# Optimization experiments

Hardware: AMD Instinct MI355X
Metric: run time of the kernel (lower is better)

Reference implementation:

```python
import jax, jax.numpy as jnp
import numpy as np

N_NODES = 100000
N_EDGES = 1000000
HID = 128


def setup_inputs() -> dict:
    key = jax.random.key(0)
    ks = jax.random.split(key, 8)
    z = jax.random.normal(ks[0], (N_NODES, HID), dtype=jnp.float32)
    edge_index = jax.random.randint(ks[1], (2, N_EDGES), 0, N_NODES, dtype=jnp.int64)
    # Linear params: W stored as [out, in] like torch; init ~ kaiming-uniform-ish scale
    W1 = jax.random.normal(ks[2], (256, 2 * HID), dtype=jnp.float32) * (1.0 / np.sqrt(2 * HID))
    b1 = jnp.zeros((256,), dtype=jnp.float32)
    W2 = jax.random.normal(ks[3], (64, 256), dtype=jnp.float32) * (1.0 / np.sqrt(256))
    b2 = jnp.zeros((64,), dtype=jnp.float32)
    W3 = jax.random.normal(ks[4], (1, 64), dtype=jnp.float32) * (1.0 / np.sqrt(64))
    b3 = jnp.zeros((1,), dtype=jnp.float32)
    return {"z": z, "edge_index": edge_index, "W1": W1, "b1": b1,
            "W2": W2, "b2": b2, "W3": W3, "b3": b3}


def reference(z, edge_index, W1, b1, W2, b2, W3, b3):
    # gather src/dst node embeddings and concat -> [E, 2*HID]
    src = z[edge_index[0]]
    dst = z[edge_index[1]]
    edge_feats = jnp.concatenate([src, dst], axis=1)
    # 3-layer MLP with leaky_relu(0.2); dropout is identity in eval mode
    h = jax.nn.leaky_relu(edge_feats @ W1.T + b1, negative_slope=0.2)
    h = jax.nn.leaky_relu(h @ W2.T + b2, negative_slope=0.2)
    return h @ W3.T + b3  # [E, 1]
```

## Files before the change

kernel.cpp:

```cpp
#include <hip/hip_runtime.h>
#include <hip/hip_bf16.h>

typedef __attribute__((ext_vector_type(8))) short bf16x8;
typedef __attribute__((ext_vector_type(4))) float f32x4;

#define HID    128
#define KDIM   256
#define MT     64

__device__ __forceinline__ unsigned short f2bf(float x) {
    unsigned int u = __float_as_uint(x);
    u += 0x7FFFu + ((u >> 16) & 1u);
    return (unsigned short)(u >> 16);
}
__device__ __forceinline__ int pack2(float a, float b) {
    return (int)f2bf(a) | ((int)f2bf(b) << 16);
}
__device__ __forceinline__ float lrelu(float x) { return fmaxf(x, 0.2f * x); }

__global__ void convert_all_kernel(const float* __restrict__ z,
                                   const float* __restrict__ W1,
                                   const float* __restrict__ W2,
                                   unsigned short* __restrict__ zb,
                                   unsigned short* __restrict__ w1b,
                                   unsigned short* __restrict__ w2b,
                                   int nz4, int nw14, int nw24) {
    int total = nz4 + nw14 + nw24;
    for (int i = blockIdx.x * blockDim.x + threadIdx.x; i < total;
         i += gridDim.x * blockDim.x) {
        const float4* src;
        unsigned short* dst;
        int j;
        if (i < nz4)             { src = (const float4*)z;  dst = zb;  j = i; }
        else if (i < nz4 + nw14) { src = (const float4*)W1; dst = w1b; j = i - nz4; }
        else                     { src = (const float4*)W2; dst = w2b; j = i - nz4 - nw14; }
        float4 v = src[j];
        ushort4 o;
        o.x = f2bf(v.x); o.y = f2bf(v.y); o.z = f2bf(v.z); o.w = f2bf(v.w);
        *(ushort4*)(dst + (size_t)j * 4) = o;
    }
}

__global__ void convert_w_kernel(const float* __restrict__ W1,
                                 const float* __restrict__ W2,
                                 unsigned short* __restrict__ w1b,
                                 unsigned short* __restrict__ w2b,
                                 int nw14, int nw24) {
    int i = blockIdx.x * blockDim.x + threadIdx.x;
    if (i >= nw14 + nw24) return;
    const float4* src;
    unsigned short* dst;
    int j;
    if (i < nw14) { src = (const float4*)W1; dst = w1b; j = i; }
    else          { src = (const float4*)W2; dst = w2b; j = i - nw14; }
    float4 v = src[j];
    ushort4 o;
    o.x = f2bf(v.x); o.y = f2bf(v.y); o.z = f2bf(v.z); o.w = f2bf(v.w);
    *(ushort4*)(dst + (size_t)j * 4) = o;
}

template <bool ZB>
__global__ __launch_bounds__(256, 4)
void disc_kernel(const float* __restrict__ z,
                 const unsigned short* __restrict__ zb,
                 const int* __restrict__ ei,
                 const unsigned short* __restrict__ w1b,
                 const float* __restrict__ b1,
                 const unsigned short* __restrict__ w2b,
                 const float* __restrict__ b2,
                 const float* __restrict__ W3,
                 const float* __restrict__ b3,
                 float* __restrict__ out, int E) {
    __shared__ __align__(16) unsigned char smem[32768];

    const int tid  = threadIdx.x;
    const int wave = tid >> 6;
    const int lane = tid & 63;
    const int lr   = lane & 15;
    const int lk   = lane >> 4;
    const int e0   = blockIdx.x * MT;

    if constexpr (ZB) {
        #pragma unroll
        for (int t = 0; t < 8; ++t) {
            int row = wave * 16 + t * 2 + (lane >> 5);
            int e = e0 + row; if (e >= E) e = E - 1;
            int s = ei[e];
            int d = ei[E + e];
            int c = (lane & 31) ^ (row & 7);
            int node = (c < 16) ? s : d;
            const unsigned short* g = zb + (size_t)node * HID + (c & 15) * 8;
            __builtin_amdgcn_global_load_lds(
                (const __attribute__((address_space(1))) unsigned int*)g,
                (__attribute__((address_space(3))) unsigned int*)(smem + wave * 8192 + t * 1024),
                16, 0, 0);
        }
    } else {
        int r = tid >> 2, q = tid & 3;
        int e = e0 + r; if (e >= E) e = E - 1;
        int s = ei[e];
        int d = ei[E + e];
        const float4* zs = (const float4*)(z + (size_t)s * HID);
        const float4* zd = (const float4*)(z + (size_t)d * HID);
        const int swz = (r & 7) << 4;
        #pragma unroll
        for (int j = 0; j < 8; ++j) {
            int c = q * 8 + j;
            const float4* src = (c < 16) ? (zs + c * 2) : (zd + (c - 16) * 2);
            float4 v0 = src[0], v1 = src[1];
            int4 o;
            o.x = pack2(v0.x, v0.y);
            o.y = pack2(v0.z, v0.w);
            o.z = pack2(v1.x, v1.y);
            o.w = pack2(v1.z, v1.w);
            *(int4*)(smem + r * 512 + ((c * 16) ^ swz)) = o;
        }
    }
    __syncthreads();

    f32x4 acc[4][4];
    #pragma unroll
    for (int mi = 0; mi < 4; ++mi)
        #pragma unroll
        for (int ni = 0; ni < 4; ++ni)
            acc[mi][ni] = (f32x4){0.f, 0.f, 0.f, 0.f};

    const int n0 = wave * 64;
    #pragma unroll
    for (int ks = 0; ks < 8; ++ks) {
        const int kb = ks * 64 + lk * 16;
        bf16x8 a[4], b[4];
        #pragma unroll
        for (int mi = 0; mi < 4; ++mi) {
            int row = mi * 16 + lr;
            a[mi] = *(const bf16x8*)(smem + row * 512 + (kb ^ ((row & 7) << 4)));
        }
        #pragma unroll
        for (int ni = 0; ni < 4; ++ni) {
            int col = n0 + ni * 16 + lr;
            b[ni] = *(const bf16x8*)(w1b + (size_t)col * KDIM + ks * 32 + lk * 8);
        }
        #pragma unroll
        for (int mi = 0; mi < 4; ++mi)
            #pragma unroll
            for (int ni = 0; ni < 4; ++ni)
                acc[mi][ni] = __builtin_amdgcn_mfma_f32_16x16x32_bf16(
                    b[ni], a[mi], acc[mi][ni], 0, 0, 0);
    }
    __syncthreads();

    #pragma unroll
    for (int ni = 0; ni < 4; ++ni) {
        int colb = n0 + ni * 16 + lk * 4;
        float4 bias = *(const float4*)(b1 + colb);
        #pragma unroll
        for (int mi = 0; mi < 4; ++mi) {
            int row = mi * 16 + lr;
            float x0 = lrelu(acc[mi][ni][0] + bias.x);
            float x1 = lrelu(acc[mi][ni][1] + bias.y);
            float x2 = lrelu(acc[mi][ni][2] + bias.z);
            float x3 = lrelu(acc[mi][ni][3] + bias.w);
            int2 o;
            o.x = pack2(x0, x1);
            o.y = pack2(x2, x3);
            *(int2*)(smem + row * 512 + ((colb * 2) ^ ((row & 7) << 4))) = o;
        }
    }
    __syncthreads();

    f32x4 acc2[4];
    #pragma unroll
    for (int mi = 0; mi < 4; ++mi) acc2[mi] = (f32x4){0.f, 0.f, 0.f, 0.f};
    const int c2 = wave * 16 + lr;
    #pragma unroll
    for (int ks = 0; ks < 8; ++ks) {
        const int kb = ks * 64 + lk * 16;
        bf16x8 a2[4];
        #pragma unroll
        for (int mi = 0; mi < 4; ++mi) {
            int row = mi * 16 + lr;
            a2[mi] = *(const bf16x8*)(smem + row * 512 + (kb ^ ((row & 7) << 4)));
        }
        bf16x8 bw = *(const bf16x8*)(w2b + (size_t)c2 * KDIM + ks * 32 + lk * 8);
        #pragma unroll
        for (int mi = 0; mi < 4; ++mi)
            acc2[mi] = __builtin_amdgcn_mfma_f32_16x16x32_bf16(
                bw, a2[mi], acc2[mi], 0, 0, 0);
    }
    __syncthreads();

    float* part = (float*)smem;
    {
        int colb = wave * 16 + lk * 4;
        float4 b2v = *(const float4*)(b2 + colb);
        float4 w3v = *(const float4*)(W3 + colb);
        #pragma unroll
        for (int mi = 0; mi < 4; ++mi) {
            float s = lrelu(acc2[mi][0] + b2v.x) * w3v.x
                    + lrelu(acc2[mi][1] + b2v.y) * w3v.y
                    + lrelu(acc2[mi][2] + b2v.z) * w3v.z
                    + lrelu(acc2[mi][3] + b2v.w) * w3v.w;
            s += __shfl_xor(s, 16);
            s += __shfl_xor(s, 32);
            if (lk == 0) part[wave * 64 + mi * 16 + lr] = s;
        }
    }
    __syncthreads();

    if (tid < MT) {
        int e = e0 + tid;
        float s = part[tid] + part[64 + tid] + part[128 + tid] + part[192 + tid] + b3[0];
        if (e < E) out[e] = s;
    }
}

extern "C" void kernel_launch(void* const* d_in, const int* in_sizes, int n_in,
                              void* d_out, int out_size, void* d_ws, size_t ws_size,
                              hipStream_t stream) {
    const float* z  = (const float*)d_in[0];
    const int*   ei = (const int*)d_in[1];
    const float* W1 = (const float*)d_in[2];
    const float* b1 = (const float*)d_in[3];
    const float* W2 = (const float*)d_in[4];
    const float* b2 = (const float*)d_in[5];
    const float* W3 = (const float*)d_in[6];
    const float* b3 = (const float*)d_in[7];
    float* out = (float*)d_out;

    const int nz  = in_sizes[0];
    const int E   = in_sizes[1] / 2;
    const int nw1 = in_sizes[2];
    const int nw2 = in_sizes[4];

    const size_t need_full = (size_t)(nz + nw1 + nw2) * 2;
    const bool zb_ok = ws_size >= need_full;

    const int blocks = (E + MT - 1) / MT;

    if (zb_ok) {
        unsigned short* zbp = (unsigned short*)d_ws;
        unsigned short* w1b = zbp + nz;
        unsigned short* w2b = w1b + nw1;
        convert_all_kernel<<<2048, 256, 0, stream>>>(z, W1, W2, zbp, w1b, w2b,
                                                     nz / 4, nw1 / 4, nw2 / 4);
        disc_kernel<true><<<blocks, 256, 0, stream>>>(z, zbp, ei, w1b, b1, w2b,
                                                      b2, W3, b3, out, E);
    } else {
        unsigned short* w1b = (unsigned short*)d_ws;
        unsigned short* w2b = w1b + nw1;
        const int ntot = (nw1 + nw2) / 4;
        convert_w_kernel<<<(ntot + 255) / 256, 256, 0, stream>>>(W1, W2, w1b, w2b,
                                                                 nw1 / 4, nw2 / 4);
        disc_kernel<false><<<blocks, 256, 0, stream>>>(z, (const unsigned short*)nullptr,
                                                       ei, w1b, b1, w2b, b2, W3, b3,
                                                       out, E);
    }
}
```

Before: 441.4 us.

## Load gathered node embeddings directly into MFMA registers, skipping LDS staging

```diff
diff --git a/kernel.cpp b/kernel.cpp
--- a/kernel.cpp
+++ b/kernel.cpp
@@ -71,7 +71,7 @@
                  const float* __restrict__ W3,
                  const float* __restrict__ b3,
                  float* __restrict__ out, int E) {
-    __shared__ __align__(16) unsigned char smem[32768];
+    __shared__ __align__(16) unsigned char smem[33792];
 
     const int tid  = threadIdx.x;
     const int wave = tid >> 6;
@@ -79,44 +79,16 @@
     const int lr   = lane & 15;
     const int lk   = lane >> 4;
     const int e0   = blockIdx.x * MT;
-
-    if constexpr (ZB) {
-        #pragma unroll
-        for (int t = 0; t < 8; ++t) {
-            int row = wave * 16 + t * 2 + (lane >> 5);
-            int e = e0 + row; if (e >= E) e = E - 1;
-            int s = ei[e];
-            int d = ei[E + e];
-            int c = (lane & 31) ^ (row & 7);
-            int node = (c < 16) ? s : d;
-            const unsigned short* g = zb + (size_t)node * HID + (c & 15) * 8;
-            __builtin_amdgcn_global_load_lds(
-                (const __attribute__((address_space(1))) unsigned int*)g,
-                (__attribute__((address_space(3))) unsigned int*)(smem + wave * 8192 + t * 1024),
-                16, 0, 0);
-        }
-    } else {
-        int r = tid >> 2, q = tid & 3;
-        int e = e0 + r; if (e >= E) e = E - 1;
-        int s = ei[e];
-        int d = ei[E + e];
-        const float4* zs = (const float4*)(z + (size_t)s * HID);
-        const float4* zd = (const float4*)(z + (size_t)d * HID);
-        const int swz = (r & 7) << 4;
-        #pragma unroll
-        for (int j = 0; j < 8; ++j) {
-            int c = q * 8 + j;
-            const float4* src = (c < 16) ? (zs + c * 2) : (zd + (c - 16) * 2);
-            float4 v0 = src[0], v1 = src[1];
-            int4 o;
-            o.x = pack2(v0.x, v0.y);
-            o.y = pack2(v0.z, v0.w);
-            o.z = pack2(v1.x, v1.y);
-            o.w = pack2(v1.z, v1.w);
-            *(int4*)(smem + r * 512 + ((c * 16) ^ swz)) = o;
-        }
-    }
-    __syncthreads();
+    const float b3s = b3[0];
+
+    unsigned soff[4], doff[4];
+    #pragma unroll
+    for (int mi = 0; mi < 4; ++mi) {
+        int e = e0 + mi * 16 + lr;
+        if (e >= E) e = E - 1;
+        soff[mi] = (unsigned)ei[e]     * HID + lk * 8;
+        doff[mi] = (unsigned)ei[E + e] * HID + lk * 8;
+    }
 
     f32x4 acc[4][4];
     #pragma unroll
@@ -126,20 +98,31 @@
             acc[mi][ni] = (f32x4){0.f, 0.f, 0.f, 0.f};
 
     const int n0 = wave * 64;
+    const unsigned short* wb = w1b + (size_t)(n0 + lr) * KDIM + lk * 8;
+
     #pragma unroll
     for (int ks = 0; ks < 8; ++ks) {
-        const int kb = ks * 64 + lk * 16;
         bf16x8 a[4], b[4];
         #pragma unroll
         for (int mi = 0; mi < 4; ++mi) {
-            int row = mi * 16 + lr;
-            a[mi] = *(const bf16x8*)(smem + row * 512 + (kb ^ ((row & 7) << 4)));
-        }
-        #pragma unroll
-        for (int ni = 0; ni < 4; ++ni) {
-            int col = n0 + ni * 16 + lr;
-            b[ni] = *(const bf16x8*)(w1b + (size_t)col * KDIM + ks * 32 + lk * 8);
-        }
+            unsigned off = ((ks < 4) ? soff[mi] : doff[mi]) + (ks & 3) * 32;
+            if constexpr (ZB) {
+                a[mi] = *(const bf16x8*)(zb + off);
+            } else {
+                const float* zp = z + off;
+                float4 v0 = *(const float4*)(zp);
+                float4 v1 = *(const float4*)(zp + 4);
+                int4 o;
+                o.x = pack2(v0.x, v0.y);
+                o.y = pack2(v0.z, v0.w);
+                o.z = pack2(v1.x, v1.y);
+                o.w = pack2(v1.z, v1.w);
+                a[mi] = *(bf16x8*)&o;
+            }
+        }
+        #pragma unroll
+        for (int ni = 0; ni < 4; ++ni)
+            b[ni] = *(const bf16x8*)(wb + (size_t)ni * 16 * KDIM + ks * 32);
         #pragma unroll
         for (int mi = 0; mi < 4; ++mi)
             #pragma unroll
@@ -147,7 +130,6 @@
                 acc[mi][ni] = __builtin_amdgcn_mfma_f32_16x16x32_bf16(
                     b[ni], a[mi], acc[mi][ni], 0, 0, 0);
     }
-    __syncthreads();
 
     #pragma unroll
     for (int ni = 0; ni < 4; ++ni) {
@@ -172,6 +154,7 @@
     #pragma unroll
     for (int mi = 0; mi < 4; ++mi) acc2[mi] = (f32x4){0.f, 0.f, 0.f, 0.f};
     const int c2 = wave * 16 + lr;
+    const unsigned short* w2base = w2b + (size_t)c2 * KDIM + lk * 8;
     #pragma unroll
     for (int ks = 0; ks < 8; ++ks) {
         const int kb = ks * 64 + lk * 16;
@@ -181,15 +164,14 @@
             int row = mi * 16 + lr;
             a2[mi] = *(const bf16x8*)(smem + row * 512 + (kb ^ ((row & 7) << 4)));
         }
-        bf16x8 bw = *(const bf16x8*)(w2b + (size_t)c2 * KDIM + ks * 32 + lk * 8);
+        bf16x8 bw = *(const bf16x8*)(w2base + ks * 32);
         #pragma unroll
         for (int mi = 0; mi < 4; ++mi)
             acc2[mi] = __builtin_amdgcn_mfma_f32_16x16x32_bf16(
                 bw, a2[mi], acc2[mi], 0, 0, 0);
     }
-    __syncthreads();
-
-    float* part = (float*)smem;
+
+    float* part = (float*)(smem + 32768);
     {
         int colb = wave * 16 + lk * 4;
         float4 b2v = *(const float4*)(b2 + colb);
@@ -209,7 +191,7 @@
 
     if (tid < MT) {
         int e = e0 + tid;
-        float s = part[tid] + part[64 + tid] + part[128 + tid] + part[192 + tid] + b3[0];
+        float s = part[tid] + part[64 + tid] + part[128 + tid] + part[192 + tid] + b3s;
         if (e < E) out[e] = s;
     }
 }
```

New measurement: 611.7 us. 38.6% more time.

## Split each 64-edge tile across 8 waves in a 2x4 wave grid

Applied to the files above, without the earlier changes.

```diff
diff --git a/kernel.cpp b/kernel.cpp
--- a/kernel.cpp
+++ b/kernel.cpp
@@ -60,7 +60,7 @@
 }
 
 template <bool ZB>
-__global__ __launch_bounds__(256, 4)
+__global__ __launch_bounds__(512, 6)
 void disc_kernel(const float* __restrict__ z,
                  const unsigned short* __restrict__ zb,
                  const int* __restrict__ ei,
@@ -71,7 +71,7 @@
                  const float* __restrict__ W3,
                  const float* __restrict__ b3,
                  float* __restrict__ out, int E) {
-    __shared__ __align__(16) unsigned char smem[32768];
+    __shared__ __align__(16) unsigned char smem[33792];
 
     const int tid  = threadIdx.x;
     const int wave = tid >> 6;
@@ -79,11 +79,12 @@
     const int lr   = lane & 15;
     const int lk   = lane >> 4;
     const int e0   = blockIdx.x * MT;
+    const float b3s = b3[0];
 
     if constexpr (ZB) {
         #pragma unroll
-        for (int t = 0; t < 8; ++t) {
-            int row = wave * 16 + t * 2 + (lane >> 5);
+        for (int t = 0; t < 4; ++t) {
+            int row = wave * 8 + t * 2 + (lane >> 5);
             int e = e0 + row; if (e >= E) e = E - 1;
             int s = ei[e];
             int d = ei[E + e];
@@ -92,11 +93,11 @@
             const unsigned short* g = zb + (size_t)node * HID + (c & 15) * 8;
             __builtin_amdgcn_global_load_lds(
                 (const __attribute__((address_space(1))) unsigned int*)g,
-                (__attribute__((address_space(3))) unsigned int*)(smem + wave * 8192 + t * 1024),
+                (__attribute__((address_space(3))) unsigned int*)(smem + wave * 4096 + t * 1024),
                 16, 0, 0);
         }
     } else {
-        int r = tid >> 2, q = tid & 3;
+        int r = tid >> 3, q = tid & 7;
         int e = e0 + r; if (e >= E) e = E - 1;
         int s = ei[e];
         int d = ei[E + e];
@@ -104,8 +105,8 @@
         const float4* zd = (const float4*)(z + (size_t)d * HID);
         const int swz = (r & 7) << 4;
         #pragma unroll
-        for (int j = 0; j < 8; ++j) {
-            int c = q * 8 + j;
+        for (int j = 0; j < 4; ++j) {
+            int c = q * 4 + j;
             const float4* src = (c < 16) ? (zs + c * 2) : (zd + (c - 16) * 2);
             float4 v0 = src[0], v1 = src[1];
             int4 o;
@@ -118,30 +119,34 @@
     }
     __syncthreads();
 
-    f32x4 acc[4][4];
-    #pragma unroll
-    for (int mi = 0; mi < 4; ++mi)
+    const int wr = wave >> 2;
+    const int wc = wave & 3;
+    const int m0 = wr * 32;
+    const int n0 = wc * 64;
+
+    f32x4 acc[2][4];
+    #pragma unroll
+    for (int mi = 0; mi < 2; ++mi)
         #pragma unroll
         for (int ni = 0; ni < 4; ++ni)
             acc[mi][ni] = (f32x4){0.f, 0.f, 0.f, 0.f};
 
-    const int n0 = wave * 64;
+    const unsigned short* wb = w1b + (size_t)(n0 + lr) * KDIM + lk * 8;
+
     #pragma unroll
     for (int ks = 0; ks < 8; ++ks) {
         const int kb = ks * 64 + lk * 16;
-        bf16x8 a[4], b[4];
-        #pragma unroll
-        for (int mi = 0; mi < 4; ++mi) {
-            int row = mi * 16 + lr;
+        bf16x8 a[2], b[4];
+        #pragma unroll
+        for (int ni = 0; ni < 4; ++ni)
+            b[ni] = *(const bf16x8*)(wb + (size_t)ni * 16 * KDIM + ks * 32);
+        #pragma unroll
+        for (int mi = 0; mi < 2; ++mi) {
+            int row = m0 + mi * 16 + lr;
             a[mi] = *(const bf16x8*)(smem + row * 512 + (kb ^ ((row & 7) << 4)));
         }
         #pragma unroll
-        for (int ni = 0; ni < 4; ++ni) {
-            int col = n0 + ni * 16 + lr;
-            b[ni] = *(const bf16x8*)(w1b + (size_t)col * KDIM + ks * 32 + lk * 8);
-        }
-        #pragma unroll
-        for (int mi = 0; mi < 4; ++mi)
+        for (int mi = 0; mi < 2; ++mi)
             #pragma unroll
             for (int ni = 0; ni < 4; ++ni)
                 acc[mi][ni] = __builtin_amdgcn_mfma_f32_16x16x32_bf16(
@@ -154,8 +159,8 @@
         int colb = n0 + ni * 16 + lk * 4;
         float4 bias = *(const float4*)(b1 + colb);
         #pragma unroll
-        for (int mi = 0; mi < 4; ++mi) {
-            int row = mi * 16 + lr;
+        for (int mi = 0; mi < 2; ++mi) {
+            int row = m0 + mi * 16 + lr;
             float x0 = lrelu(acc[mi][ni][0] + bias.x);
             float x1 = lrelu(acc[mi][ni][1] + bias.y);
             float x2 = lrelu(acc[mi][ni][2] + bias.z);
@@ -168,48 +173,49 @@
     }
     __syncthreads();
 
-    f32x4 acc2[4];
-    #pragma unroll
-    for (int mi = 0; mi < 4; ++mi) acc2[mi] = (f32x4){0.f, 0.f, 0.f, 0.f};
-    const int c2 = wave * 16 + lr;
+    f32x4 acc2[2];
+    acc2[0] = (f32x4){0.f, 0.f, 0.f, 0.f};
+    acc2[1] = (f32x4){0.f, 0.f, 0.f, 0.f};
+    const int c2 = wc * 16 + lr;
+    const unsigned short* w2base = w2b + (size_t)c2 * KDIM + lk * 8;
     #pragma unroll
     for (int ks = 0; ks < 8; ++ks) {
         const int kb = ks * 64 + lk * 16;
-        bf16x8 a2[4];
-        #pragma unroll
-        for (int mi = 0; mi < 4; ++mi) {
-            int row = mi * 16 + lr;
+        bf16x8 a2[2];
+        #pragma unroll
+        for (int mi = 0; mi < 2; ++mi) {
+            int row = m0 + mi * 16 + lr;
             a2[mi] = *(const bf16x8*)(smem + row * 512 + (kb ^ ((row & 7) << 4)));
         }
-        bf16x8 bw = *(const bf16x8*)(w2b + (size_t)c2 * KDIM + ks * 32 + lk * 8);
-        #pragma unroll
-        for (int mi = 0; mi < 4; ++mi)
+        bf16x8 bw = *(const bf16x8*)(w2base + ks * 32);
+        #pragma unroll
+        for (int mi = 0; mi < 2; ++mi)
             acc2[mi] = __builtin_amdgcn_mfma_f32_16x16x32_bf16(
                 bw, a2[mi], acc2[mi], 0, 0, 0);
     }
     __syncthreads();
 
-    float* part = (float*)smem;
+    float* part = (float*)(smem + 32768);
     {
-        int colb = wave * 16 + lk * 4;
+        int colb = wc * 16 + lk * 4;
         float4 b2v = *(const float4*)(b2 + colb);
         float4 w3v = *(const float4*)(W3 + colb);
         #pragma unroll
-        for (int mi = 0; mi < 4; ++mi) {
+        for (int mi = 0; mi < 2; ++mi) {
             float s = lrelu(acc2[mi][0] + b2v.x) * w3v.x
                     + lrelu(acc2[mi][1] + b2v.y) * w3v.y
                     + lrelu(acc2[mi][2] + b2v.z) * w3v.z
                     + lrelu(acc2[mi][3] + b2v.w) * w3v.w;
             s += __shfl_xor(s, 16);
             s += __shfl_xor(s, 32);
-            if (lk == 0) part[wave * 64 + mi * 16 + lr] = s;
+            if (lk == 0) part[wc * 64 + m0 + mi * 16 + lr] = s;
         }
     }
     __syncthreads();
 
     if (tid < MT) {
         int e = e0 + tid;
-        float s = part[tid] + part[64 + tid] + part[128 + tid] + part[192 + tid] + b3[0];
+        float s = part[tid] + part[64 + tid] + part[128 + tid] + part[192 + tid] + b3s;
         if (e < E) out[e] = s;
     }
 }
@@ -243,7 +249,7 @@
         unsigned short* w2b = w1b + nw1;
         convert_all_kernel<<<2048, 256, 0, stream>>>(z, W1, W2, zbp, w1b, w2b,
                                                      nz / 4, nw1 / 4, nw2 / 4);
-        disc_kernel<true><<<blocks, 256, 0, stream>>>(z, zbp, ei, w1b, b1, w2b,
+        disc_kernel<true><<<blocks, 512, 0, stream>>>(z, zbp, ei, w1b, b1, w2b,
                                                       b2, W3, b3, out, E);
     } else {
         unsigned short* w1b = (unsigned short*)d_ws;
@@ -251,7 +257,7 @@
         const int ntot = (nw1 + nw2) / 4;
         convert_w_kernel<<<(ntot + 255) / 256, 256, 0, stream>>>(W1, W2, w1b, w2b,
                                                                  nw1 / 4, nw2 / 4);
-        disc_kernel<false><<<blocks, 256, 0, stream>>>(z, (const unsigned short*)nullptr,
+        disc_kernel<false><<<blocks, 512, 0, stream>>>(z, (const unsigned short*)nullptr,
                                                        ei, w1b, b1, w2b, b2, W3, b3,
                                                        out, E);
     }
```

After: 687.1 us. 1.56x slower.
